# Performance work log

Measured on AMD Instinct MI355X. Metric: run time of the kernel, lower is better.

## Reference

```python
import jax, jax.numpy as jnp
import numpy as np

B, D, L, H = 2048, 64, 64, 512  # batch, in_dim, latent_space, hidden


def setup_inputs() -> dict:
    key = jax.random.key(0)
    ks = jax.random.split(key, 12)
    inp = {
        "x": jax.random.normal(ks[0], (B, D), jnp.float32),
        "koopman": jax.random.normal(ks[1], (B, L, D), jnp.float32),
    }
    dims = [(L, H), (H, H), (H, H), (H, D)]
    k = 2
    for pfx in ("s", "t"):
        for j, (fi, fo) in enumerate(dims):
            inp[f"{pfx}W{j+1}"] = jax.random.normal(ks[k], (fi, fo), jnp.float32) / np.sqrt(fi).astype(np.float32)
            inp[f"{pfx}b{j+1}"] = jnp.zeros((fo,), jnp.float32)
            k += 1
    return inp


def _mlp(z, W1, b1, W2, b2, W3, b3, W4, b4):
    h = jnp.tanh(z @ W1 + b1)
    h = jnp.tanh(h @ W2 + b2)
    h = jnp.tanh(h @ W3 + b3)
    return h @ W4 + b4


def reference(x, koopman,
              sW1, sb1, sW2, sb2, sW3, sb3, sW4, sb4,
              tW1, tb1, tW2, tb2, tW3, tb3, tW4, tb4):
    # koopman: (B, L, D) -> z: (B, D, L); column i of the torch loop is z[:, i, :]
    z = jnp.swapaxes(koopman, 1, 2)
    s = _mlp(z, sW1, sb1, sW2, sb2, sW3, sb3, sW4, sb4)  # (B, D, D)
    t = _mlp(z, tW1, tb1, tW2, tb2, tW3, tb3, tW4, tb4)  # (B, D, D)
    # loop kept only output column i for input column i -> diagonal over last two dims
    ds = jnp.diagonal(s, axis1=1, axis2=2)  # (B, D)
    dt = jnp.diagonal(t, axis1=1, axis2=2)  # (B, D)
    return (x - dt) * jnp.exp(-ds)
```

## Files before the change

### kernel.cpp

```cpp
#include <hip/hip_runtime.h>


typedef _Float16 f16;
typedef _Float16 f16x8 __attribute__((ext_vector_type(8)));
typedef float f32x16 __attribute__((ext_vector_type(16)));

#define WPACK_PER_NET 589824
#define OFF_W1 0
#define OFF_W2 32768
#define OFF_W3 294912
#define OFF_W4T 557056
#define WPACK_BYTES (2u * WPACK_PER_NET * sizeof(f16))

__global__ void pack_weights(const float* __restrict__ sW1, const float* __restrict__ sW2,
                             const float* __restrict__ sW3, const float* __restrict__ sW4,
                             const float* __restrict__ tW1, const float* __restrict__ tW2,
                             const float* __restrict__ tW3, const float* __restrict__ tW4,
                             f16* __restrict__ dst) {
  int idx8 = (blockIdx.x * 256 + threadIdx.x) * 8;
  if (idx8 >= 2 * WPACK_PER_NET) return;
  int net = idx8 >= WPACK_PER_NET;
  int f = idx8 - net * WPACK_PER_NET;
  const float* W1 = net ? tW1 : sW1;
  const float* W2 = net ? tW2 : sW2;
  const float* W3 = net ? tW3 : sW3;
  const float* W4 = net ? tW4 : sW4;
  f16x8 o;
  if (f < OFF_W2) {
    int lane = (f >> 3) & 63, ctg = (f >> 9) & 15, ks = f >> 13;
    int r0 = ks * 16 + (lane >> 5) * 8, c = ctg * 32 + (lane & 31);
#pragma unroll
    for (int j = 0; j < 8; j++) o[j] = (f16)W1[(r0 + j) * 512 + c];
  } else if (f < OFF_W3) {
    int f2 = f - OFF_W2;
    int lane = (f2 >> 3) & 63, ctg = (f2 >> 9) & 15, ks = f2 >> 13;
    int r0 = ks * 16 + (lane >> 5) * 8, c = ctg * 32 + (lane & 31);
#pragma unroll
    for (int j = 0; j < 8; j++) o[j] = (f16)W2[(r0 + j) * 512 + c];
  } else if (f < OFF_W4T) {
    int f3 = f - OFF_W3;
    int lane = (f3 >> 3) & 63, ctg = (f3 >> 9) & 15, ks = f3 >> 13;
    int r0 = ks * 16 + (lane >> 5) * 8, c = ctg * 32 + (lane & 31);
#pragma unroll
    for (int j = 0; j < 8; j++) o[j] = (f16)W3[(r0 + j) * 512 + c];
  } else {
    int f4 = f - OFF_W4T;
    int i = f4 >> 9, k0 = f4 & 511;
#pragma unroll
    for (int j = 0; j < 8; j++) o[j] = (f16)W4[(k0 + j) * 64 + i];
  }
  *(f16x8*)(dst + net * WPACK_PER_NET + f) = o;
}

__device__ __forceinline__ int aidx(int m, int k) {
  return ((k >> 4) * 2 + (m >> 5)) * 512 + ((m & 31) + 32 * ((k >> 3) & 1)) * 8 + (k & 7);
}

__device__ __forceinline__ int swz(int e) {
  return e ^ (((e >> 8) & 1) << 3) ^ (((e >> 10) & 1) << 4);
}

__device__ __forceinline__ float fast_tanh(float x) {
  float e = __expf(x + x);
  return fmaf(-2.0f, __builtin_amdgcn_rcpf(e + 1.0f), 1.0f);
}

template <bool PACKED>
__device__ __forceinline__ void load_b(const f16* __restrict__ Wblk,
                                       const float* __restrict__ Wraw,
                                       int ks, int wave, int lane, f16x8* bdst) {
  if (PACKED) {
#pragma unroll
    for (int ct = 0; ct < 2; ct++)
      bdst[ct] = *(const f16x8*)(Wblk + ((ks * 16 + wave * 2 + ct) * 64 + lane) * 8);
  } else {
    int r0 = ks * 16 + (lane >> 5) * 8;
    int n0 = wave * 64 + (lane & 31);
#pragma unroll
    for (int ct = 0; ct < 2; ct++) {
      f16x8 v;
#pragma unroll
      for (int j = 0; j < 8; j++) v[j] = (f16)Wraw[(r0 + j) * 512 + n0 + ct * 32];
      bdst[ct] = v;
    }
  }
}

template <int NS, bool PACKED, bool ALIASED>
__device__ __forceinline__ void mlp_layer(const f16* __restrict__ Wblk,
                                          const float* __restrict__ Wraw,
                                          const float* __restrict__ bias,
                                          const f16* Asrc, f16* Hout,
                                          int wave, int lane, int sbase,
                                          int lane8s, int lane_m) {
  f32x16 acc[2][2];
#pragma unroll
  for (int ct = 0; ct < 2; ct++) {
    float bv = bias[wave * 64 + ct * 32 + (lane & 31)];
#pragma unroll
    for (int mt = 0; mt < 2; mt++)
#pragma unroll
      for (int e = 0; e < 16; e++) acc[mt][ct][e] = bv;
  }

  const f16* abE = Asrc + lane8s;
  const f16* abO = Asrc + (lane8s ^ 16);

  f16x8 bb[2][2];
  load_b<PACKED>(Wblk, Wraw, 0, wave, lane, bb[0]);
#pragma unroll
  for (int ks = 0; ks < NS; ks++) {
    if (ks + 1 < NS) load_b<PACKED>(Wblk, Wraw, ks + 1, wave, lane, bb[(ks + 1) & 1]);
    const f16* ab = ((ks & 1) ? abO : abE) + ks * 1024;
    f16x8 a0 = *(const f16x8*)ab;
    f16x8 a1 = *(const f16x8*)(ab + 512);
#pragma unroll
    for (int ct = 0; ct < 2; ct++) {
      acc[0][ct] = __builtin_amdgcn_mfma_f32_32x32x16_f16(a0, bb[ks & 1][ct],
                                                          acc[0][ct], 0, 0, 0);
      acc[1][ct] = __builtin_amdgcn_mfma_f32_32x32x16_f16(a1, bb[ks & 1][ct],
                                                          acc[1][ct], 0, 0, 0);
    }
  }
  if (ALIASED) __syncthreads();

#pragma unroll
  for (int rr = 0; rr < 4; rr++) {
    f16* hb = Hout + sbase + ((rr ^ lane_m) << 3);
#pragma unroll
    for (int mt = 0; mt < 2; mt++)
#pragma unroll
      for (int ct = 0; ct < 2; ct++)
#pragma unroll
        for (int rq = 0; rq < 4; rq++)
          hb[ct * 2048 + mt * 512 + rq * 64] =
              (f16)fast_tanh(acc[mt][ct][rq * 4 + rr]);
  }
  __syncthreads();
}

template <bool PACKED>
__global__ __launch_bounds__(512, 4) void decoder_main(
    const float* __restrict__ x, const float* __restrict__ koop,
    const f16* __restrict__ wpack,
    const float* __restrict__ sW1, const float* __restrict__ sW2,
    const float* __restrict__ sW3, const float* __restrict__ sW4,
    const float* __restrict__ tW1, const float* __restrict__ tW2,
    const float* __restrict__ tW3, const float* __restrict__ tW4,
    const float* __restrict__ sb1, const float* __restrict__ sb2,
    const float* __restrict__ sb3, const float* __restrict__ sb4,
    const float* __restrict__ tb1, const float* __restrict__ tb2,
    const float* __restrict__ tb3, const float* __restrict__ tb4,
    float* __restrict__ out) {
  __shared__ __align__(16) f16 ZA[4096];
  __shared__ __align__(16) f16 HA[32768];
  __shared__ float pp[512];
  __shared__ float redBuf[2][64];

  const int b = blockIdx.x;
  const int t = threadIdx.x;
  const int wave = t >> 6, lane = t & 63;
  const int sbase = wave * 4096 + ((lane >> 4) & 1) * 1024 +
                    ((lane >> 3) & 1) * 256 + (lane >> 5) * 32 + (lane & 7);
  const int lane8s = (lane * 8) ^ (((lane >> 5) & 1) << 3);
  const int lane_m = ((lane >> 3) & 1) | (((lane >> 4) & 1) << 1);

  const float* kb = koop + b * 4096;
#pragma unroll
  for (int i = 0; i < 8; i++) {
    int flat = t + 512 * i;
    ZA[swz(aidx(flat & 63, flat >> 6))] = (f16)kb[flat];
  }
  __syncthreads();

  for (int net = 0; net < 2; net++) {
    const f16* wb = PACKED ? (wpack + net * WPACK_PER_NET) : (const f16*)0;
    const float* W1 = net ? tW1 : sW1;
    const float* W2 = net ? tW2 : sW2;
    const float* W3 = net ? tW3 : sW3;
    const float* W4 = net ? tW4 : sW4;
    const float* b1 = net ? tb1 : sb1;
    const float* b2 = net ? tb2 : sb2;
    const float* b3 = net ? tb3 : sb3;
    const float* b4 = net ? tb4 : sb4;
    mlp_layer<4, PACKED, false>(PACKED ? wb + OFF_W1 : 0, W1, b1, ZA, HA,
                                wave, lane, sbase, lane8s, lane_m);
    mlp_layer<32, PACKED, true>(PACKED ? wb + OFF_W2 : 0, W2, b2, HA, HA,
                                wave, lane, sbase, lane8s, lane_m);
    mlp_layer<32, PACKED, true>(PACKED ? wb + OFF_W3 : 0, W3, b3, HA, HA,
                                wave, lane, sbase, lane8s, lane_m);

    {
      int i = lane, oct = wave;
      float p = 0.f;
#pragma unroll
      for (int q = 0; q < 8; q++) {
        int k0 = oct * 64 + q * 8;
        f16x8 hv = *(const f16x8*)&HA[swz(aidx(i, k0))];
#pragma unroll
        for (int j = 0; j < 8; j++)
          p += (float)hv[j] * W4[(k0 + j) * 64 + i];
      }
      pp[oct * 64 + i] = p;
    }
    __syncthreads();
    if (t < 64) {
      float s = b4[t];
#pragma unroll
      for (int o = 0; o < 8; o++) s += pp[o * 64 + t];
      redBuf[net][t] = s;
    }
    __syncthreads();
  }

  if (t < 64) {
    out[b * 64 + t] = (x[b * 64 + t] - redBuf[1][t]) * __expf(-redBuf[0][t]);
  }
}

extern "C" void kernel_launch(void* const* d_in, const int* in_sizes, int n_in,
                              void* d_out, int out_size, void* d_ws, size_t ws_size,
                              hipStream_t stream) {
  const float* x    = (const float*)d_in[0];
  const float* koop = (const float*)d_in[1];
  const float* sW1 = (const float*)d_in[2];  const float* sb1 = (const float*)d_in[3];
  const float* sW2 = (const float*)d_in[4];  const float* sb2 = (const float*)d_in[5];
  const float* sW3 = (const float*)d_in[6];  const float* sb3 = (const float*)d_in[7];
  const float* sW4 = (const float*)d_in[8];  const float* sb4 = (const float*)d_in[9];
  const float* tW1 = (const float*)d_in[10]; const float* tb1 = (const float*)d_in[11];
  const float* tW2 = (const float*)d_in[12]; const float* tb2 = (const float*)d_in[13];
  const float* tW3 = (const float*)d_in[14]; const float* tb3 = (const float*)d_in[15];
  const float* tW4 = (const float*)d_in[16]; const float* tb4 = (const float*)d_in[17];
  float* out = (float*)d_out;

  if (ws_size >= (size_t)WPACK_BYTES) {
    f16* wpack = (f16*)d_ws;
    pack_weights<<<576, 256, 0, stream>>>(sW1, sW2, sW3, sW4, tW1, tW2, tW3, tW4, wpack);
    decoder_main<true><<<2048, 512, 0, stream>>>(
        x, koop, wpack, sW1, sW2, sW3, sW4, tW1, tW2, tW3, tW4,
        sb1, sb2, sb3, sb4, tb1, tb2, tb3, tb4, out);
  } else {
    decoder_main<false><<<2048, 512, 0, stream>>>(
        x, koop, (const f16*)0, sW1, sW2, sW3, sW4, tW1, tW2, tW3, tW4,
        sb1, sb2, sb3, sb4, tb1, tb2, tb3, tb4, out);
  }
}
```

Baseline: 462.0 us.

## Swap MFMA operand roles so weights feed A and activations stored transposed

Computes each layer as the transposed product (W^T times activations^T), so packed weights become the MFMA A operand and activations are read as B from a transposed LDS layout without XOR swizzling. Bias is now added after accumulation using vectorized float4 loads, and outputs are written to LDS as 4-wide f16 vectors instead of scalar stores. The aim is fewer, wider LDS writes and simpler addressing. The cost is possible LDS bank conflicts now that the swizzle is gone.

Measured after the change: 468.3 us. About the same (+1.4%).

```diff
diff --git a/kernel.cpp b/kernel.cpp
--- a/kernel.cpp
+++ b/kernel.cpp
@@ -2,6 +2,7 @@
 
 
 typedef _Float16 f16;
+typedef _Float16 f16x4 __attribute__((ext_vector_type(4)));
 typedef _Float16 f16x8 __attribute__((ext_vector_type(8)));
 typedef float f32x16 __attribute__((ext_vector_type(16)));
 
@@ -27,20 +28,20 @@
   const float* W4 = net ? tW4 : sW4;
   f16x8 o;
   if (f < OFF_W2) {
-    int lane = (f >> 3) & 63, ctg = (f >> 9) & 15, ks = f >> 13;
-    int r0 = ks * 16 + (lane >> 5) * 8, c = ctg * 32 + (lane & 31);
+    int lane = (f >> 3) & 63, g = (f >> 9) & 15, ks = f >> 13;
+    int r0 = ks * 16 + (lane >> 5) * 8, c = g * 32 + (lane & 31);
 #pragma unroll
     for (int j = 0; j < 8; j++) o[j] = (f16)W1[(r0 + j) * 512 + c];
   } else if (f < OFF_W3) {
     int f2 = f - OFF_W2;
-    int lane = (f2 >> 3) & 63, ctg = (f2 >> 9) & 15, ks = f2 >> 13;
-    int r0 = ks * 16 + (lane >> 5) * 8, c = ctg * 32 + (lane & 31);
+    int lane = (f2 >> 3) & 63, g = (f2 >> 9) & 15, ks = f2 >> 13;
+    int r0 = ks * 16 + (lane >> 5) * 8, c = g * 32 + (lane & 31);
 #pragma unroll
     for (int j = 0; j < 8; j++) o[j] = (f16)W2[(r0 + j) * 512 + c];
   } else if (f < OFF_W4T) {
     int f3 = f - OFF_W3;
-    int lane = (f3 >> 3) & 63, ctg = (f3 >> 9) & 15, ks = f3 >> 13;
-    int r0 = ks * 16 + (lane >> 5) * 8, c = ctg * 32 + (lane & 31);
+    int lane = (f3 >> 3) & 63, g = (f3 >> 9) & 15, ks = f3 >> 13;
+    int r0 = ks * 16 + (lane >> 5) * 8, c = g * 32 + (lane & 31);
 #pragma unroll
     for (int j = 0; j < 8; j++) o[j] = (f16)W3[(r0 + j) * 512 + c];
   } else {
@@ -52,12 +53,8 @@
   *(f16x8*)(dst + net * WPACK_PER_NET + f) = o;
 }
 
-__device__ __forceinline__ int aidx(int m, int k) {
-  return ((k >> 4) * 2 + (m >> 5)) * 512 + ((m & 31) + 32 * ((k >> 3) & 1)) * 8 + (k & 7);
-}
-
-__device__ __forceinline__ int swz(int e) {
-  return e ^ (((e >> 8) & 1) << 3) ^ (((e >> 10) & 1) << 4);
+__device__ __forceinline__ int zbidx(int k, int j) {
+  return ((k >> 4) * 2 + (j >> 5)) * 512 + ((j & 31) + 32 * ((k >> 3) & 1)) * 8 + (k & 7);
 }
 
 __device__ __forceinline__ float fast_tanh(float x) {
@@ -66,22 +63,22 @@
 }
 
 template <bool PACKED>
-__device__ __forceinline__ void load_b(const f16* __restrict__ Wblk,
+__device__ __forceinline__ void load_a(const f16* __restrict__ Wblk,
                                        const float* __restrict__ Wraw,
-                                       int ks, int wave, int lane, f16x8* bdst) {
+                                       int ks, int wave, int lane, f16x8* adst) {
   if (PACKED) {
 #pragma unroll
-    for (int ct = 0; ct < 2; ct++)
-      bdst[ct] = *(const f16x8*)(Wblk + ((ks * 16 + wave * 2 + ct) * 64 + lane) * 8);
+    for (int it = 0; it < 2; it++)
+      adst[it] = *(const f16x8*)(Wblk + ((ks * 16 + wave * 2 + it) * 64 + lane) * 8);
   } else {
     int r0 = ks * 16 + (lane >> 5) * 8;
     int n0 = wave * 64 + (lane & 31);
 #pragma unroll
-    for (int ct = 0; ct < 2; ct++) {
+    for (int it = 0; it < 2; it++) {
       f16x8 v;
 #pragma unroll
-      for (int j = 0; j < 8; j++) v[j] = (f16)Wraw[(r0 + j) * 512 + n0 + ct * 32];
-      bdst[ct] = v;
+      for (int j = 0; j < 8; j++) v[j] = (f16)Wraw[(r0 + j) * 512 + n0 + it * 32];
+      adst[it] = v;
     }
   }
 }
@@ -90,52 +87,61 @@
 __device__ __forceinline__ void mlp_layer(const f16* __restrict__ Wblk,
                                           const float* __restrict__ Wraw,
                                           const float* __restrict__ bias,
-                                          const f16* Asrc, f16* Hout,
-                                          int wave, int lane, int sbase,
-                                          int lane8s, int lane_m) {
+                                          const f16* Bsrc, f16* Tout,
+                                          int wave, int lane) {
   f32x16 acc[2][2];
 #pragma unroll
-  for (int ct = 0; ct < 2; ct++) {
-    float bv = bias[wave * 64 + ct * 32 + (lane & 31)];
-#pragma unroll
-    for (int mt = 0; mt < 2; mt++)
-#pragma unroll
-      for (int e = 0; e < 16; e++) acc[mt][ct][e] = bv;
-  }
-
-  const f16* abE = Asrc + lane8s;
-  const f16* abO = Asrc + (lane8s ^ 16);
-
-  f16x8 bb[2][2];
-  load_b<PACKED>(Wblk, Wraw, 0, wave, lane, bb[0]);
+  for (int it = 0; it < 2; it++)
+#pragma unroll
+    for (int jt = 0; jt < 2; jt++)
+#pragma unroll
+      for (int e = 0; e < 16; e++) acc[it][jt][e] = 0.f;
+
+  f16x8 aw[2][2];
+  load_a<PACKED>(Wblk, Wraw, 0, wave, lane, aw[0]);
 #pragma unroll
   for (int ks = 0; ks < NS; ks++) {
-    if (ks + 1 < NS) load_b<PACKED>(Wblk, Wraw, ks + 1, wave, lane, bb[(ks + 1) & 1]);
-    const f16* ab = ((ks & 1) ? abO : abE) + ks * 1024;
-    f16x8 a0 = *(const f16x8*)ab;
-    f16x8 a1 = *(const f16x8*)(ab + 512);
-#pragma unroll
-    for (int ct = 0; ct < 2; ct++) {
-      acc[0][ct] = __builtin_amdgcn_mfma_f32_32x32x16_f16(a0, bb[ks & 1][ct],
-                                                          acc[0][ct], 0, 0, 0);
-      acc[1][ct] = __builtin_amdgcn_mfma_f32_32x32x16_f16(a1, bb[ks & 1][ct],
-                                                          acc[1][ct], 0, 0, 0);
-    }
-  }
+    if (ks + 1 < NS) load_a<PACKED>(Wblk, Wraw, ks + 1, wave, lane, aw[(ks + 1) & 1]);
+    const f16* bb = Bsrc + ks * 1024 + lane * 8;
+    f16x8 b0 = *(const f16x8*)bb;
+    f16x8 b1 = *(const f16x8*)(bb + 512);
+#pragma unroll
+    for (int it = 0; it < 2; it++) {
+      acc[it][0] = __builtin_amdgcn_mfma_f32_32x32x16_f16(aw[ks & 1][it], b0,
+                                                          acc[it][0], 0, 0, 0);
+      acc[it][1] = __builtin_amdgcn_mfma_f32_32x32x16_f16(aw[ks & 1][it], b1,
+                                                          acc[it][1], 0, 0, 0);
+    }
+  }
+
+  const int h = lane >> 5;
+  f16x4 hv[2][2][4];
+#pragma unroll
+  for (int it = 0; it < 2; it++)
+#pragma unroll
+    for (int rq = 0; rq < 4; rq++) {
+      float4 bv = *(const float4*)&bias[wave * 64 + it * 32 + rq * 8 + h * 4];
+#pragma unroll
+      for (int jt = 0; jt < 2; jt++) {
+        f16x4 v;
+#pragma unroll
+        for (int rr = 0; rr < 4; rr++)
+          v[rr] = (f16)fast_tanh(acc[it][jt][rq * 4 + rr] + (&bv.x)[rr]);
+        hv[it][jt][rq] = v;
+      }
+    }
+
   if (ALIASED) __syncthreads();
 
-#pragma unroll
-  for (int rr = 0; rr < 4; rr++) {
-    f16* hb = Hout + sbase + ((rr ^ lane_m) << 3);
-#pragma unroll
-    for (int mt = 0; mt < 2; mt++)
-#pragma unroll
-      for (int ct = 0; ct < 2; ct++)
-#pragma unroll
-        for (int rq = 0; rq < 4; rq++)
-          hb[ct * 2048 + mt * 512 + rq * 64] =
-              (f16)fast_tanh(acc[mt][ct][rq * 4 + rr]);
-  }
+  f16* wb = Tout + wave * 4096 + (lane & 31) * 8 + 4 * h;
+#pragma unroll
+  for (int it = 0; it < 2; it++)
+#pragma unroll
+    for (int jt = 0; jt < 2; jt++)
+#pragma unroll
+      for (int rq = 0; rq < 4; rq++)
+        *(f16x4*)(wb + it * 2048 + jt * 512 + (rq >> 1) * 1024 + (rq & 1) * 256) =
+            hv[it][jt][rq];
   __syncthreads();
 }
 
@@ -152,7 +158,7 @@
     const float* __restrict__ tb1, const float* __restrict__ tb2,
     const float* __restrict__ tb3, const float* __restrict__ tb4,
     float* __restrict__ out) {
-  __shared__ __align__(16) f16 ZA[4096];
+  __shared__ __align__(16) f16 ZB[4096];
   __shared__ __align__(16) f16 HA[32768];
   __shared__ float pp[512];
   __shared__ float redBuf[2][64];
@@ -160,16 +166,12 @@
   const int b = blockIdx.x;
   const int t = threadIdx.x;
   const int wave = t >> 6, lane = t & 63;
-  const int sbase = wave * 4096 + ((lane >> 4) & 1) * 1024 +
-                    ((lane >> 3) & 1) * 256 + (lane >> 5) * 32 + (lane & 7);
-  const int lane8s = (lane * 8) ^ (((lane >> 5) & 1) << 3);
-  const int lane_m = ((lane >> 3) & 1) | (((lane >> 4) & 1) << 1);
 
   const float* kb = koop + b * 4096;
 #pragma unroll
   for (int i = 0; i < 8; i++) {
     int flat = t + 512 * i;
-    ZA[swz(aidx(flat & 63, flat >> 6))] = (f16)kb[flat];
+    ZB[zbidx(flat >> 6, flat & 63)] = (f16)kb[flat];
   }
   __syncthreads();
 
@@ -183,25 +185,21 @@
     const float* b2 = net ? tb2 : sb2;
     const float* b3 = net ? tb3 : sb3;
     const float* b4 = net ? tb4 : sb4;
-    mlp_layer<4, PACKED, false>(PACKED ? wb + OFF_W1 : 0, W1, b1, ZA, HA,
-                                wave, lane, sbase, lane8s, lane_m);
-    mlp_layer<32, PACKED, true>(PACKED ? wb + OFF_W2 : 0, W2, b2, HA, HA,
-                                wave, lane, sbase, lane8s, lane_m);
-    mlp_layer<32, PACKED, true>(PACKED ? wb + OFF_W3 : 0, W3, b3, HA, HA,
-                                wave, lane, sbase, lane8s, lane_m);
+    mlp_layer<4, PACKED, false>(PACKED ? wb + OFF_W1 : 0, W1, b1, ZB, HA, wave, lane);
+    mlp_layer<32, PACKED, true>(PACKED ? wb + OFF_W2 : 0, W2, b2, HA, HA, wave, lane);
+    mlp_layer<32, PACKED, true>(PACKED ? wb + OFF_W3 : 0, W3, b3, HA, HA, wave, lane);
 
     {
-      int i = lane, oct = wave;
       float p = 0.f;
 #pragma unroll
       for (int q = 0; q < 8; q++) {
-        int k0 = oct * 64 + q * 8;
-        f16x8 hv = *(const f16x8*)&HA[swz(aidx(i, k0))];
+        int k0 = wave * 64 + q * 8;
+        f16x8 hv = *(const f16x8*)&HA[zbidx(k0, lane)];
 #pragma unroll
         for (int j = 0; j < 8; j++)
-          p += (float)hv[j] * W4[(k0 + j) * 64 + i];
+          p += (float)hv[j] * W4[(k0 + j) * 64 + lane];
       }
-      pp[oct * 64 + i] = p;
+      pp[wave * 64 + lane] = p;
     }
     __syncthreads();
     if (t < 64) {
```
